# Optimization experiments

Hardware: AMD Instinct MI355X
Metric: run time of the kernel (lower is better)

The kernel has to match this reference:

```python
import jax, jax.numpy as jnp
import numpy as np
from jax import lax

NPOINT = 1024
NSAMPLE = 32
EPS = 1e-5


def setup_inputs() -> dict:
    key = jax.random.key(0)
    ks = jax.random.split(key, 8)
    B, N, CF = 16, 4096, 64
    xyz = jax.random.normal(ks[0], (B, N, 3), jnp.float32)
    points = jax.random.normal(ks[1], (B, N, CF), jnp.float32)
    in_ch = 3 + CF
    # 1x1 Conv2d weights stored as (out_ch, in_ch); kaiming-ish scale
    w0 = jax.random.normal(ks[2], (64, in_ch), jnp.float32) / np.sqrt(in_ch)
    w1 = jax.random.normal(ks[3], (64, 64), jnp.float32) / np.sqrt(64)
    w2 = jax.random.normal(ks[4], (128, 64), jnp.float32) / np.sqrt(64)
    z64 = jnp.zeros((64,), jnp.float32)
    z128 = jnp.zeros((128,), jnp.float32)
    o64 = jnp.ones((64,), jnp.float32)
    o128 = jnp.ones((128,), jnp.float32)
    return {
        "xyz": xyz, "points": points,
        "w0": w0, "b0": z64, "g0": o64, "bb0": z64,
        "w1": w1, "b1": z64, "g1": o64, "bb1": z64,
        "w2": w2, "b2": z128, "g2": o128, "bb2": z128,
    }


def _fps(xyz, npoint):
    """Iterative farthest point sampling. xyz: (B,N,3) -> (B,npoint) int32.
    Deterministic start at index 0 (torch uses a random start)."""
    B, N, _ = xyz.shape

    def step(carry, _):
        distance, farthest = carry
        centroid = jnp.take_along_axis(xyz, farthest[:, None, None], axis=1)  # (B,1,3)
        dist = jnp.sum((xyz - centroid) ** 2, -1)  # (B,N)
        distance = jnp.minimum(distance, dist)
        new_far = jnp.argmax(distance, axis=-1).astype(jnp.int32)
        return (distance, new_far), farthest

    init = (jnp.full((B, N), 1e10, xyz.dtype), jnp.zeros((B,), jnp.int32))
    _, cents = lax.scan(step, init, None, length=npoint)  # (npoint, B)
    return cents.T  # (B, npoint)


def _gather(pts, idx):
    """pts: (B,N,C), idx: (B,S,K) -> (B,S,K,C)"""
    return jax.vmap(lambda p, i: p[i])(pts, idx)


def _bn_relu(x, g, b):
    # training-mode BatchNorm over all axes except channel (last), biased var
    mean = jnp.mean(x, axis=(0, 1, 2))
    var = jnp.var(x, axis=(0, 1, 2))
    return jax.nn.relu(g * (x - mean) * lax.rsqrt(var + EPS) + b)


def reference(xyz, points, w0, b0, g0, bb0, w1, b1, g1, bb1, w2, b2, g2, bb2):
    B, N, _ = xyz.shape
    fps_idx = _fps(xyz, NPOINT)  # (B,S)
    new_xyz = jnp.take_along_axis(xyz, fps_idx[..., None], axis=1)  # (B,S,3)
    # squared distances centroid->all points: (B,S,N)
    d2 = (jnp.sum(new_xyz ** 2, -1)[:, :, None]
          + jnp.sum(xyz ** 2, -1)[:, None, :]
          - 2.0 * jnp.einsum("bsc,bnc->bsn", new_xyz, xyz))
    _, idx = lax.top_k(-d2, NSAMPLE)  # (B,S,K) nearest-K (sort-based ball query)
    grouped_xyz = _gather(xyz, idx) - new_xyz[:, :, None, :]  # (B,S,K,3)
    grouped_pts = _gather(points, idx)  # (B,S,K,CF)
    h = jnp.concatenate([grouped_xyz, grouped_pts], axis=-1)  # (B,S,K,3+CF)
    for w, b, g, bb in ((w0, b0, g0, bb0), (w1, b1, g1, bb1), (w2, b2, g2, bb2)):
        h = _bn_relu(jnp.einsum("bskc,oc->bsko", h, w) + b, g, bb)
    new_points = jnp.max(h, axis=2)  # (B,S,C_out) max over K
    new_points = jnp.transpose(new_points, (0, 2, 1))  # (B,C_out,S) matches torch
    return new_xyz, new_points
```

## Files before the change

### kernel.cpp

```cpp
#include <hip/hip_runtime.h>
#include <hip/hip_bf16.h>

#define NB 16
#define NN 4096
#define NS 1024
#define NK 32
#define CF 64
#define CIN 67
#define MTOT 524288
#define NEWP_OFF 49152

__device__ inline unsigned bf16bits(float v) {
    __hip_bfloat16 h = __float2bfloat16(v);
    unsigned short s;
    __builtin_memcpy(&s, &h, 2);
    return (unsigned)s;
}
__device__ inline float4 ldY4(const float* p) { return *(const float4*)p; }
__device__ inline float4 ldY4(const __hip_bfloat16* p) {
    ushort4 u = *(const ushort4*)p;
    return make_float4(__uint_as_float((unsigned)u.x << 16),
                       __uint_as_float((unsigned)u.y << 16),
                       __uint_as_float((unsigned)u.z << 16),
                       __uint_as_float((unsigned)u.w << 16));
}
__device__ inline void stY2(float* p, float a, float b) { *(float2*)p = make_float2(a, b); }
__device__ inline void stY2(__hip_bfloat16* p, float a, float b) {
    *(unsigned*)p = bf16bits(a) | (bf16bits(b) << 16);
}

template <int CTRL>
__device__ inline float dppredmax(float v) {
    int j = __builtin_amdgcn_update_dpp(__float_as_int(v), __float_as_int(v),
                                        CTRL, 0xF, 0xF, false);
    return fmaxf(v, __int_as_float(j));
}
template <int CTRL>
__device__ inline float dppredmin(float v) {
    int j = __builtin_amdgcn_update_dpp(__float_as_int(v), __float_as_int(v),
                                        CTRL, 0xF, 0xF, false);
    return fminf(v, __int_as_float(j));
}
template <int CTRL>
__device__ inline float dppadd0(float v) {
    int j = __builtin_amdgcn_update_dpp(0, __float_as_int(v), CTRL, 0xF, 0xF, true);
    return __fadd_rn(v, __int_as_float(j));
}
template <int CTRL>
__device__ inline unsigned long long dppredmin64(unsigned long long v) {
    int lo = (int)(unsigned)(v & 0xffffffffULL), hi = (int)(unsigned)(v >> 32);
    unsigned nlo = (unsigned)__builtin_amdgcn_update_dpp(lo, lo, CTRL, 0xF, 0xF, false);
    unsigned nhi = (unsigned)__builtin_amdgcn_update_dpp(hi, hi, CTRL, 0xF, 0xF, false);
    unsigned long long o = ((unsigned long long)nhi << 32) | nlo;
    return o < v ? o : v;
}
__device__ inline float wavemax_to_all(float tmax) {
    float g = tmax;
    g = dppredmax<0x111>(g);
    g = dppredmax<0x112>(g);
    g = dppredmax<0x114>(g);
    g = dppredmax<0x118>(g);
    g = dppredmax<0x142>(g);
    g = dppredmax<0x143>(g);
    return __int_as_float(__builtin_amdgcn_readlane(__float_as_int(g), 63));
}
__device__ inline unsigned long long wavemin64_to_all(unsigned long long v) {
    v = dppredmin64<0x111>(v);
    v = dppredmin64<0x112>(v);
    v = dppredmin64<0x114>(v);
    v = dppredmin64<0x118>(v);
    v = dppredmin64<0x142>(v);
    v = dppredmin64<0x143>(v);
    unsigned lo = (unsigned)__builtin_amdgcn_readlane((int)(unsigned)(v & 0xffffffffULL), 63);
    unsigned hi = (unsigned)__builtin_amdgcn_readlane((int)(unsigned)(v >> 32), 63);
    return ((unsigned long long)hi << 32) | lo;
}
__device__ inline float wavesum64(float v) {
    v = dppadd0<0x111>(v); v = dppadd0<0x112>(v);
    v = dppadd0<0x114>(v); v = dppadd0<0x118>(v);
    v = dppadd0<0x142>(v); v = dppadd0<0x143>(v);
    return v;
}
__device__ inline float segmax16(float v) {
    v = dppredmax<0x111>(v); v = dppredmax<0x112>(v);
    v = dppredmax<0x114>(v); v = dppredmax<0x118>(v);
    return v;
}
__device__ inline float segmin16(float v) {
    v = dppredmin<0x111>(v); v = dppredmin<0x112>(v);
    v = dppredmin<0x114>(v); v = dppredmin<0x118>(v);
    return v;
}

__global__ __launch_bounds__(256) void fps_kernel(const float* __restrict__ xyz,
                                                  int* __restrict__ fps_idx) {
    __shared__ float4 cpt[NN];
    __shared__ unsigned long long part[2][4];
    const int b = blockIdx.x, t = threadIdx.x;
    const float4* src = (const float4*)(xyz + (size_t)b * NN * 3);
    float px[16], py[16], pz[16], dist[16];
#pragma unroll
    for (int j = 0; j < 4; ++j) {
        float4 A = src[t * 12 + 3 * j], B4 = src[t * 12 + 3 * j + 1], C4 = src[t * 12 + 3 * j + 2];
        px[4 * j + 0] = A.x;  py[4 * j + 0] = A.y;  pz[4 * j + 0] = A.z;
        px[4 * j + 1] = A.w;  py[4 * j + 1] = B4.x; pz[4 * j + 1] = B4.y;
        px[4 * j + 2] = B4.z; py[4 * j + 2] = B4.w; pz[4 * j + 2] = C4.x;
        px[4 * j + 3] = C4.y; py[4 * j + 3] = C4.z; pz[4 * j + 3] = C4.w;
    }
#pragma unroll
    for (int i = 0; i < 16; ++i) {
        dist[i] = 1e10f;
        cpt[16 * t + i] = make_float4(px[i], py[i], pz[i], 0.f);
    }
    __syncthreads();
    int cur = 0;
    float4 c = cpt[0];
    const int wv = t >> 6;
    for (int s = 0; s < NS; ++s) {
        if (t == 0) fps_idx[(b << 10) + s] = cur;
#pragma unroll
        for (int i = 0; i < 16; ++i) {
            float dx = __fsub_rn(px[i], c.x), dy = __fsub_rn(py[i], c.y), dz = __fsub_rn(pz[i], c.z);
            float d = __fadd_rn(__fadd_rn(__fmul_rn(dx, dx), __fmul_rn(dy, dy)), __fmul_rn(dz, dz));
            dist[i] = fminf(dist[i], d);
        }
        float m0 = fmaxf(dist[0], dist[1]),   m1 = fmaxf(dist[2], dist[3]);
        float m2 = fmaxf(dist[4], dist[5]),   m3 = fmaxf(dist[6], dist[7]);
        float m4 = fmaxf(dist[8], dist[9]),   m5 = fmaxf(dist[10], dist[11]);
        float m6 = fmaxf(dist[12], dist[13]), m7 = fmaxf(dist[14], dist[15]);
        m0 = fmaxf(m0, m1); m2 = fmaxf(m2, m3); m4 = fmaxf(m4, m5); m6 = fmaxf(m6, m7);
        m0 = fmaxf(m0, m2); m4 = fmaxf(m4, m6);
        const float tmax = fmaxf(m0, m4);
        int mi = 15;
#pragma unroll
        for (int i = 14; i >= 0; --i) mi = (dist[i] == tmax) ? i : mi;
        const float gmax = wavemax_to_all(tmax);
        unsigned long long mask = __ballot(tmax == gmax);
        int ldr = __ffsll(mask) - 1;
        int widx = __builtin_amdgcn_readlane(16 * t + mi, ldr);
        if ((t & 63) == 0) {
            part[s & 1][wv] =
                ((unsigned long long)__float_as_uint(gmax) << 32) | (unsigned)(4095 - widx);
        }
        __syncthreads();
        unsigned long long k0 = part[s & 1][0], k1 = part[s & 1][1];
        unsigned long long k2 = part[s & 1][2], k3 = part[s & 1][3];
        unsigned long long ka = k0 > k1 ? k0 : k1, kb = k2 > k3 ? k2 : k3;
        unsigned long long k = ka > kb ? ka : kb;
        cur = 4095 - (int)(unsigned)(k & 0xffffffffu);
        c = cpt[cur];
    }
}

__global__ __launch_bounds__(256) void knn_kernel(const float* __restrict__ xyz,
                                                  const int* __restrict__ fps_idx,
                                                  int* __restrict__ knn,
                                                  float* __restrict__ out) {
    __shared__ float4 cpt[NN];
    const int b = blockIdx.x >> 5, cb = blockIdx.x & 31, t = threadIdx.x;
    for (int p = t; p < NN; p += 256) {
        const float* xr = xyz + ((size_t)(b << 12) + p) * 3;
        float x = xr[0], y = xr[1], z = xr[2];
        float pn = __fadd_rn(__fadd_rn(__fmul_rn(x, x), __fmul_rn(y, y)), __fmul_rn(z, z));
        cpt[p] = make_float4(x, y, z, pn);
    }
    __syncthreads();
    const int lane = t & 63, wv = t >> 6;
    for (int r = 0; r < 8; ++r) {
        const int s = (cb << 5) + (wv << 3) + r;
        const int ci = fps_idx[(b << 10) + s];
        const float4 cq = cpt[ci];
        const float cx = cq.x, cy = cq.y, cz = cq.z, cn = cq.w;
        if (lane < 3) out[((size_t)(b << 10) + s) * 3 + lane] = (lane == 0) ? cx : (lane == 1 ? cy : cz);
        unsigned long long m1 = ~0ULL, m2 = ~0ULL, m3 = ~0ULL;
#pragma unroll
        for (int i = 0; i < 64; ++i) {
            int p = lane + (i << 6);
            float4 q = cpt[p];
            float dot = __fadd_rn(__fadd_rn(__fmul_rn(cx, q.x), __fmul_rn(cy, q.y)),
                                  __fmul_rn(cz, q.z));
            float d2 = __fsub_rn(__fadd_rn(cn, q.w), __fmul_rn(2.0f, dot));
            unsigned u = __float_as_uint(d2);
            unsigned enc = u ^ ((unsigned)((int)u >> 31) | 0x80000000u);
            unsigned long long key = ((unsigned long long)enc << 32) | (unsigned)p;
            if (key < m3) {
                if (key < m1)      { m3 = m2; m2 = m1; m1 = key; }
                else if (key < m2) { m3 = m2; m2 = key; }
                else               { m3 = key; }
            }
        }
        unsigned myidx = 0;
        for (int j = 0; j < 32; ++j) {
            const unsigned long long vmin = wavemin64_to_all(m1);
            if (lane == j) myidx = (unsigned)(vmin & 0xffffffffu);
            if (m1 == vmin) {
                m1 = m2; m2 = m3; m3 = ~0ULL;
                if (m1 == ~0ULL) {
#pragma unroll
                    for (int i = 0; i < 64; ++i) {
                        int p = lane + (i << 6);
                        float4 q = cpt[p];
                        float dot = __fadd_rn(__fadd_rn(__fmul_rn(cx, q.x), __fmul_rn(cy, q.y)),
                                              __fmul_rn(cz, q.z));
                        float d2 = __fsub_rn(__fadd_rn(cn, q.w), __fmul_rn(2.0f, dot));
                        unsigned u = __float_as_uint(d2);
                        unsigned enc = u ^ ((unsigned)((int)u >> 31) | 0x80000000u);
                        unsigned long long key = ((unsigned long long)enc << 32) | (unsigned)p;
                        if (key > vmin && key < m3) {
                            if (key < m1)      { m3 = m2; m2 = m1; m1 = key; }
                            else if (key < m2) { m3 = m2; m2 = key; }
                            else               { m3 = key; }
                        }
                    }
                }
            }
        }
        const int rowbase = ((b << 10) + s) << 5;
        if (lane < 32) knn[rowbase + lane] = (int)myidx;
    }
}

template <typename YT>
__global__ __launch_bounds__(256) void conv0_kernel(
    const float* __restrict__ xyz, const float* __restrict__ points,
    const float* __restrict__ out_xyz, const int* __restrict__ knn,
    const float* __restrict__ w0, const float* __restrict__ b0,
    YT* __restrict__ Y0, float* __restrict__ gs, float* __restrict__ gq) {
    __shared__ float Ht[CIN][128];
    __shared__ float bsm[64], bqm[64];
    const int t = threadIdx.x;
    const int eb = blockIdx.x << 7;
    {
        const int le = t >> 1, part = t & 1;
        const int e = eb + le;
        const int b = e >> 15, s = (e >> 5) & 1023;
        const int pidx = knn[e];
        const float4* pr = (const float4*)(points + (((size_t)(b << 12) + pidx) << 6)) + (part << 3);
        if (part == 0) {
            const float* xr = xyz + ((size_t)(b << 12) + pidx) * 3;
            const float* cr = out_xyz + ((size_t)(b << 10) + s) * 3;
            Ht[0][le] = xr[0] - cr[0];
            Ht[1][le] = xr[1] - cr[1];
            Ht[2][le] = xr[2] - cr[2];
        }
#pragma unroll
        for (int q = 0; q < 8; ++q) {
            float4 v = pr[q];
            int c = 3 + (part << 5) + (q << 2);
            Ht[c][le] = v.x; Ht[c + 1][le] = v.y; Ht[c + 2][le] = v.z; Ht[c + 3][le] = v.w;
        }
    }
    __syncthreads();
    const int wvu = __builtin_amdgcn_readfirstlane(t >> 6);
    const int lane = t & 63, e2 = (t & 63) << 1;
    const float* __restrict__ wrow = w0 + (wvu << 4) * CIN;
    float acc[16][2];
#pragma unroll
    for (int i = 0; i < 16; ++i) { acc[i][0] = 0.f; acc[i][1] = 0.f; }
#pragma unroll 2
    for (int c = 0; c < CIN; ++c) {
        const float2 a = *(const float2*)&Ht[c][e2];
#pragma unroll
        for (int i = 0; i < 16; ++i) {
            const float w = wrow[i * CIN + c];
            acc[i][0] += w * a.x;
            acc[i][1] += w * a.y;
        }
    }
    const int o0 = wvu << 4;
#pragma unroll
    for (int i = 0; i < 16; ++i) {
        const float bi = b0[o0 + i];
        const float v0 = acc[i][0] + bi, v1 = acc[i][1] + bi;
        stY2(&Y0[(size_t)(o0 + i) * MTOT + eb + e2], v0, v1);
        float ss = wavesum64(v0 + v1);
        float qq = wavesum64(v0 * v0 + v1 * v1);
        if (lane == 63) { bsm[o0 + i] = ss; bqm[o0 + i] = qq; }
    }
    __syncthreads();
    if (t < 64) atomicAdd(&gs[t], bsm[t]);
    else if (t < 128) atomicAdd(&gq[t - 64], bqm[t - 64]);
}

template <typename YT>
__global__ __launch_bounds__(256) void conv1_kernel(
    const YT* __restrict__ Y0, const float* __restrict__ w1, const float* __restrict__ b1,
    const float* __restrict__ gsp, const float* __restrict__ gqp,
    const float* __restrict__ g, const float* __restrict__ bb,
    YT* __restrict__ Y1, float* __restrict__ gs, float* __restrict__ gq) {
    __shared__ float At[64][128];
    __shared__ float bnsc[64], bnsh[64];
    __shared__ float bsm[64], bqm[64];
    const int t = threadIdx.x;
    const int eb = blockIdx.x << 7;
    if (t < 64) {
        const float inv = 1.f / (float)MTOT;
        float mean = gsp[t] * inv;
        float var = gqp[t] * inv - mean * mean;
        float r = g[t] / sqrtf(var + 1e-5f);
        bnsc[t] = r; bnsh[t] = bb[t] - mean * r;
    }
    __syncthreads();
    {
        const int c = t >> 2, base = (t & 3) << 5;
        const float sx = bnsc[c], hx = bnsh[c];
#pragma unroll
        for (int q = 0; q < 8; ++q) {
            const int col = base + (q << 2);
            float4 y = ldY4(&Y0[(size_t)c * MTOT + eb + col]);
            *(float4*)&At[c][col] = make_float4(fmaxf(sx * y.x + hx, 0.f),
                                                fmaxf(sx * y.y + hx, 0.f),
                                                fmaxf(sx * y.z + hx, 0.f),
                                                fmaxf(sx * y.w + hx, 0.f));
        }
    }
    __syncthreads();
    const int wvu = __builtin_amdgcn_readfirstlane(t >> 6);
    const int lane = t & 63, e2 = (t & 63) << 1;
    const float* __restrict__ wrow = w1 + (wvu << 4) * 64;
    float acc[16][2];
#pragma unroll
    for (int i = 0; i < 16; ++i) { acc[i][0] = 0.f; acc[i][1] = 0.f; }
#pragma unroll 2
    for (int c = 0; c < 64; ++c) {
        const float2 a = *(const float2*)&At[c][e2];
#pragma unroll
        for (int i = 0; i < 16; ++i) {
            const float w = wrow[(i << 6) + c];
            acc[i][0] += w * a.x;
            acc[i][1] += w * a.y;
        }
    }
    const int o0 = wvu << 4;
#pragma unroll
    for (int i = 0; i < 16; ++i) {
        const float bi = b1[o0 + i];
        const float v0 = acc[i][0] + bi, v1 = acc[i][1] + bi;
        stY2(&Y1[(size_t)(o0 + i) * MTOT + eb + e2], v0, v1);
        float ss = wavesum64(v0 + v1);
        float qq = wavesum64(v0 * v0 + v1 * v1);
        if (lane == 63) { bsm[o0 + i] = ss; bqm[o0 + i] = qq; }
    }
    __syncthreads();
    if (t < 64) atomicAdd(&gs[t], bsm[t]);
    else if (t < 128) atomicAdd(&gq[t - 64], bqm[t - 64]);
}

template <typename YT>
__global__ __launch_bounds__(256) void conv2s_kernel(
    const YT* __restrict__ Y1, const float* __restrict__ w2, const float* __restrict__ b2,
    const float* __restrict__ gsp, const float* __restrict__ gqp,
    const float* __restrict__ g, const float* __restrict__ bb,
    float* __restrict__ gs, float* __restrict__ gq,
    float* __restrict__ Mx, float* __restrict__ Mn) {
    __shared__ float At[64][128];
    __shared__ float bnsc[64], bnsh[64];
    __shared__ float bsm[128], bqm[128];
    __shared__ float mxs[4][128], mns[4][128];
    const int t = threadIdx.x;
    const int eb = blockIdx.x << 7;
    if (t < 64) {
        const float inv = 1.f / (float)MTOT;
        float mean = gsp[t] * inv;
        float var = gqp[t] * inv - mean * mean;
        float r = g[t] / sqrtf(var + 1e-5f);
        bnsc[t] = r; bnsh[t] = bb[t] - mean * r;
    }
    __syncthreads();
    {
        const int c = t >> 2, base = (t & 3) << 5;
        const float sx = bnsc[c], hx = bnsh[c];
#pragma unroll
        for (int q = 0; q < 8; ++q) {
            const int col = base + (q << 2);
            float4 y = ldY4(&Y1[(size_t)c * MTOT + eb + col]);
            *(float4*)&At[c][col] = make_float4(fmaxf(sx * y.x + hx, 0.f),
                                                fmaxf(sx * y.y + hx, 0.f),
                                                fmaxf(sx * y.z + hx, 0.f),
                                                fmaxf(sx * y.w + hx, 0.f));
        }
    }
    __syncthreads();
    const int wvu = __builtin_amdgcn_readfirstlane(t >> 6);
    const int lane = t & 63, e2 = (t & 63) << 1;
    const float* __restrict__ wrow = w2 + (wvu << 5) * 64;
    float acc[32][2];
#pragma unroll
    for (int i = 0; i < 32; ++i) { acc[i][0] = 0.f; acc[i][1] = 0.f; }
#pragma unroll 2
    for (int c = 0; c < 64; ++c) {
        const float2 a = *(const float2*)&At[c][e2];
#pragma unroll
        for (int i = 0; i < 32; ++i) {
            const float w = wrow[(i << 6) + c];
            acc[i][0] += w * a.x;
            acc[i][1] += w * a.y;
        }
    }
    const int o0 = wvu << 5;
    const int srow = lane >> 4;
#pragma unroll
    for (int i = 0; i < 32; ++i) {
        const float bi = b2[o0 + i];
        const float v0 = acc[i][0] + bi, v1 = acc[i][1] + bi;
        float ss = wavesum64(v0 + v1);
        float qq = wavesum64(v0 * v0 + v1 * v1);
        if (lane == 63) { bsm[o0 + i] = ss; bqm[o0 + i] = qq; }
        float mx = segmax16(fmaxf(v0, v1));
        float mn = segmin16(fminf(v0, v1));
        if ((lane & 15) == 15) { mxs[srow][o0 + i] = mx; mns[srow][o0 + i] = mn; }
    }
    __syncthreads();
    if (t < 128) atomicAdd(&gs[t], bsm[t]);
    else atomicAdd(&gq[t - 128], bqm[t - 128]);
    const int sidx0 = blockIdx.x << 2;
    for (int i = t; i < 512; i += 256) {
        int row = i >> 7, o = i & 127;
        Mx[(size_t)(sidx0 + row) * 128 + o] = mxs[row][o];
        Mn[(size_t)(sidx0 + row) * 128 + o] = mns[row][o];
    }
}

__global__ __launch_bounds__(256) void final2_kernel(
    const float* __restrict__ Mx, const float* __restrict__ Mn,
    const float* __restrict__ gsp, const float* __restrict__ gqp,
    const float* __restrict__ g, const float* __restrict__ bb,
    float* __restrict__ out) {
    __shared__ float T[128][65];
    __shared__ float bnsc[128], bnsh[128];
    const int t = threadIdx.x;
    if (t < 128) {
        const float inv = 1.f / (float)MTOT;
        float mean = gsp[t] * inv;
        float var = gqp[t] * inv - mean * mean;
        float r = g[t] / sqrtf(var + 1e-5f);
        bnsc[t] = r; bnsh[t] = bb[t] - mean * r;
    }
    __syncthreads();
    const int b = blockIdx.x >> 4, s0 = (blockIdx.x & 15) << 6;
    for (int i = t; i < 8192; i += 256) {
        int r = i >> 7, o = i & 127;
        size_t src = ((size_t)(b << 10) + s0 + r) * 128 + o;
        float a = bnsc[o];
        float m = (a >= 0.f) ? Mx[src] : Mn[src];
        T[o][r] = fmaxf(a * m + bnsh[o], 0.f);
    }
    __syncthreads();
    float* np = out + NEWP_OFF;
    for (int i = t; i < 8192; i += 256) {
        int o = i >> 6, r = i & 63;
        np[((size_t)(b << 7) + o) * 1024 + s0 + r] = T[o][r];
    }
}

extern "C" void kernel_launch(void* const* d_in, const int* in_sizes, int n_in,
                              void* d_out, int out_size, void* d_ws, size_t ws_size,
                              hipStream_t stream) {
    const float* xyz = (const float*)d_in[0];
    const float* points = (const float*)d_in[1];
    const float* w0 = (const float*)d_in[2];
    const float* b0 = (const float*)d_in[3];
    const float* g0 = (const float*)d_in[4];
    const float* bb0 = (const float*)d_in[5];
    const float* w1 = (const float*)d_in[6];
    const float* b1 = (const float*)d_in[7];
    const float* g1 = (const float*)d_in[8];
    const float* bb1 = (const float*)d_in[9];
    const float* w2 = (const float*)d_in[10];
    const float* b2 = (const float*)d_in[11];
    const float* g2 = (const float*)d_in[12];
    const float* bb2 = (const float*)d_in[13];
    float* out = (float*)d_out;
    char* ws = (char*)d_ws;

    int* knn = (int*)(ws);
    int* fps = (int*)(ws + (2u << 20));
    float* stats = (float*)(ws + (2u << 20) + (1u << 16));
    float *gs0 = stats, *gq0 = stats + 64, *gs1 = stats + 128, *gq1 = stats + 192;
    float *gs2 = stats + 256, *gq2 = stats + 384;
    float* Mx = (float*)(ws + (4ull << 20));
    float* Mn = (float*)(ws + (12ull << 20));
    const size_t yoff = 20ull << 20;
    const size_t ybytes_f32 = (size_t)MTOT * 64 * 4;
    const bool f32p = ws_size >= yoff + 2 * ybytes_f32;

    (void)hipMemsetAsync(stats, 0, 512 * sizeof(float), stream);
    fps_kernel<<<NB, 256, 0, stream>>>(xyz, fps);
    knn_kernel<<<NB * 32, 256, 0, stream>>>(xyz, fps, knn, out);

    if (f32p) {
        float* Y0 = (float*)(ws + yoff);
        float* Y1 = Y0 + (size_t)MTOT * 64;
        conv0_kernel<float><<<4096, 256, 0, stream>>>(xyz, points, out, knn, w0, b0, Y0, gs0, gq0);
        conv1_kernel<float><<<4096, 256, 0, stream>>>(Y0, w1, b1, gs0, gq0, g0, bb0, Y1, gs1, gq1);
        conv2s_kernel<float><<<4096, 256, 0, stream>>>(Y1, w2, b2, gs1, gq1, g1, bb1, gs2, gq2, Mx, Mn);
    } else {
        __hip_bfloat16* Y0 = (__hip_bfloat16*)(ws + yoff);
        __hip_bfloat16* Y1 = Y0 + (size_t)MTOT * 64;
        conv0_kernel<__hip_bfloat16><<<4096, 256, 0, stream>>>(xyz, points, out, knn, w0, b0, Y0, gs0, gq0);
        conv1_kernel<__hip_bfloat16><<<4096, 256, 0, stream>>>(Y0, w1, b1, gs0, gq0, g0, bb0, Y1, gs1, gq1);
        conv2s_kernel<__hip_bfloat16><<<4096, 256, 0, stream>>>(Y1, w2, b2, gs1, gq1, g1, bb1, gs2, gq2, Mx, Mn);
    }
    final2_kernel<<<256, 256, 0, stream>>>(Mx, Mn, gs2, gq2, g2, bb2, out);
}
```

Measured before the change: 1.313 ms.

## Process two batches per FPS block to interleave independent serial chains

The FPS kernel now runs two batch elements in one 256-thread block, launching 8 blocks instead of 16. The two independent distance updates and argmax reductions are interleaved so their latency chains overlap and they share one barrier per step. This doubles registers and LDS per block (two 64KB point buffers) and halves the number of blocks, so each step does twice the ALU work on the same CU.

```diff
diff --git a/kernel.cpp b/kernel.cpp
--- a/kernel.cpp
+++ b/kernel.cpp
@@ -92,63 +92,108 @@
     return v;
 }
 
-__global__ __launch_bounds__(256) void fps_kernel(const float* __restrict__ xyz,
-                                                  int* __restrict__ fps_idx) {
-    __shared__ float4 cpt[NN];
-    __shared__ unsigned long long part[2][4];
-    const int b = blockIdx.x, t = threadIdx.x;
-    const float4* src = (const float4*)(xyz + (size_t)b * NN * 3);
-    float px[16], py[16], pz[16], dist[16];
+__global__ __launch_bounds__(256, 1) void fps_kernel(const float* __restrict__ xyz,
+                                                     int* __restrict__ fps_idx) {
+    __shared__ float4 cptA[NN];
+    __shared__ float4 cptB[NN];
+    __shared__ unsigned long long partA[2][4], partB[2][4];
+    const int bA = blockIdx.x, bB = blockIdx.x + 8, t = threadIdx.x;
+    const float4* srcA = (const float4*)(xyz + (size_t)bA * NN * 3);
+    const float4* srcB = (const float4*)(xyz + (size_t)bB * NN * 3);
+    float pxA[16], pyA[16], pzA[16], dA[16];
+    float pxB[16], pyB[16], pzB[16], dB[16];
 #pragma unroll
     for (int j = 0; j < 4; ++j) {
-        float4 A = src[t * 12 + 3 * j], B4 = src[t * 12 + 3 * j + 1], C4 = src[t * 12 + 3 * j + 2];
-        px[4 * j + 0] = A.x;  py[4 * j + 0] = A.y;  pz[4 * j + 0] = A.z;
-        px[4 * j + 1] = A.w;  py[4 * j + 1] = B4.x; pz[4 * j + 1] = B4.y;
-        px[4 * j + 2] = B4.z; py[4 * j + 2] = B4.w; pz[4 * j + 2] = C4.x;
-        px[4 * j + 3] = C4.y; py[4 * j + 3] = C4.z; pz[4 * j + 3] = C4.w;
+        float4 A = srcA[t * 12 + 3 * j], B4 = srcA[t * 12 + 3 * j + 1], C4 = srcA[t * 12 + 3 * j + 2];
+        pxA[4 * j + 0] = A.x;  pyA[4 * j + 0] = A.y;  pzA[4 * j + 0] = A.z;
+        pxA[4 * j + 1] = A.w;  pyA[4 * j + 1] = B4.x; pzA[4 * j + 1] = B4.y;
+        pxA[4 * j + 2] = B4.z; pyA[4 * j + 2] = B4.w; pzA[4 * j + 2] = C4.x;
+        pxA[4 * j + 3] = C4.y; pyA[4 * j + 3] = C4.z; pzA[4 * j + 3] = C4.w;
+    }
+#pragma unroll
+    for (int j = 0; j < 4; ++j) {
+        float4 A = srcB[t * 12 + 3 * j], B4 = srcB[t * 12 + 3 * j + 1], C4 = srcB[t * 12 + 3 * j + 2];
+        pxB[4 * j + 0] = A.x;  pyB[4 * j + 0] = A.y;  pzB[4 * j + 0] = A.z;
+        pxB[4 * j + 1] = A.w;  pyB[4 * j + 1] = B4.x; pzB[4 * j + 1] = B4.y;
+        pxB[4 * j + 2] = B4.z; pyB[4 * j + 2] = B4.w; pzB[4 * j + 2] = C4.x;
+        pxB[4 * j + 3] = C4.y; pyB[4 * j + 3] = C4.z; pzB[4 * j + 3] = C4.w;
     }
 #pragma unroll
     for (int i = 0; i < 16; ++i) {
-        dist[i] = 1e10f;
-        cpt[16 * t + i] = make_float4(px[i], py[i], pz[i], 0.f);
-    }
-    __syncthreads();
-    int cur = 0;
-    float4 c = cpt[0];
+        dA[i] = 1e10f; dB[i] = 1e10f;
+        cptA[16 * t + i] = make_float4(pxA[i], pyA[i], pzA[i], 0.f);
+        cptB[16 * t + i] = make_float4(pxB[i], pyB[i], pzB[i], 0.f);
+    }
+    __syncthreads();
+    int curA = 0, curB = 0;
+    float4 cA = cptA[0], cB = cptB[0];
     const int wv = t >> 6;
     for (int s = 0; s < NS; ++s) {
-        if (t == 0) fps_idx[(b << 10) + s] = cur;
+        if (t == 0) {
+            fps_idx[(bA << 10) + s] = curA;
+            fps_idx[(bB << 10) + s] = curB;
+        }
 #pragma unroll
         for (int i = 0; i < 16; ++i) {
-            float dx = __fsub_rn(px[i], c.x), dy = __fsub_rn(py[i], c.y), dz = __fsub_rn(pz[i], c.z);
+            float dx = __fsub_rn(pxA[i], cA.x), dy = __fsub_rn(pyA[i], cA.y), dz = __fsub_rn(pzA[i], cA.z);
             float d = __fadd_rn(__fadd_rn(__fmul_rn(dx, dx), __fmul_rn(dy, dy)), __fmul_rn(dz, dz));
-            dist[i] = fminf(dist[i], d);
-        }
-        float m0 = fmaxf(dist[0], dist[1]),   m1 = fmaxf(dist[2], dist[3]);
-        float m2 = fmaxf(dist[4], dist[5]),   m3 = fmaxf(dist[6], dist[7]);
-        float m4 = fmaxf(dist[8], dist[9]),   m5 = fmaxf(dist[10], dist[11]);
-        float m6 = fmaxf(dist[12], dist[13]), m7 = fmaxf(dist[14], dist[15]);
-        m0 = fmaxf(m0, m1); m2 = fmaxf(m2, m3); m4 = fmaxf(m4, m5); m6 = fmaxf(m6, m7);
-        m0 = fmaxf(m0, m2); m4 = fmaxf(m4, m6);
-        const float tmax = fmaxf(m0, m4);
-        int mi = 15;
-#pragma unroll
-        for (int i = 14; i >= 0; --i) mi = (dist[i] == tmax) ? i : mi;
-        const float gmax = wavemax_to_all(tmax);
-        unsigned long long mask = __ballot(tmax == gmax);
-        int ldr = __ffsll(mask) - 1;
-        int widx = __builtin_amdgcn_readlane(16 * t + mi, ldr);
+            dA[i] = fminf(dA[i], d);
+        }
+#pragma unroll
+        for (int i = 0; i < 16; ++i) {
+            float dx = __fsub_rn(pxB[i], cB.x), dy = __fsub_rn(pyB[i], cB.y), dz = __fsub_rn(pzB[i], cB.z);
+            float d = __fadd_rn(__fadd_rn(__fmul_rn(dx, dx), __fmul_rn(dy, dy)), __fmul_rn(dz, dz));
+            dB[i] = fminf(dB[i], d);
+        }
+        float a0 = fmaxf(dA[0], dA[1]),   a1 = fmaxf(dA[2], dA[3]);
+        float a2 = fmaxf(dA[4], dA[5]),   a3 = fmaxf(dA[6], dA[7]);
+        float a4 = fmaxf(dA[8], dA[9]),   a5 = fmaxf(dA[10], dA[11]);
+        float a6 = fmaxf(dA[12], dA[13]), a7 = fmaxf(dA[14], dA[15]);
+        a0 = fmaxf(a0, a1); a2 = fmaxf(a2, a3); a4 = fmaxf(a4, a5); a6 = fmaxf(a6, a7);
+        a0 = fmaxf(a0, a2); a4 = fmaxf(a4, a6);
+        const float tmaxA = fmaxf(a0, a4);
+        int miA = 15;
+#pragma unroll
+        for (int i = 14; i >= 0; --i) miA = (dA[i] == tmaxA) ? i : miA;
+        float b0 = fmaxf(dB[0], dB[1]),   b1 = fmaxf(dB[2], dB[3]);
+        float b2 = fmaxf(dB[4], dB[5]),   b3 = fmaxf(dB[6], dB[7]);
+        float b4 = fmaxf(dB[8], dB[9]),   b5 = fmaxf(dB[10], dB[11]);
+        float b6 = fmaxf(dB[12], dB[13]), b7 = fmaxf(dB[14], dB[15]);
+        b0 = fmaxf(b0, b1); b2 = fmaxf(b2, b3); b4 = fmaxf(b4, b5); b6 = fmaxf(b6, b7);
+        b0 = fmaxf(b0, b2); b4 = fmaxf(b4, b6);
+        const float tmaxB = fmaxf(b0, b4);
+        int miB = 15;
+#pragma unroll
+        for (int i = 14; i >= 0; --i) miB = (dB[i] == tmaxB) ? i : miB;
+        const float gA = wavemax_to_all(tmaxA);
+        const float gB = wavemax_to_all(tmaxB);
+        unsigned long long mA = __ballot(tmaxA == gA);
+        unsigned long long mB = __ballot(tmaxB == gB);
+        int widxA = __builtin_amdgcn_readlane(16 * t + miA, __ffsll(mA) - 1);
+        int widxB = __builtin_amdgcn_readlane(16 * t + miB, __ffsll(mB) - 1);
         if ((t & 63) == 0) {
-            part[s & 1][wv] =
-                ((unsigned long long)__float_as_uint(gmax) << 32) | (unsigned)(4095 - widx);
+            partA[s & 1][wv] =
+                ((unsigned long long)__float_as_uint(gA) << 32) | (unsigned)(4095 - widxA);
+            partB[s & 1][wv] =
+                ((unsigned long long)__float_as_uint(gB) << 32) | (unsigned)(4095 - widxB);
         }
         __syncthreads();
-        unsigned long long k0 = part[s & 1][0], k1 = part[s & 1][1];
-        unsigned long long k2 = part[s & 1][2], k3 = part[s & 1][3];
-        unsigned long long ka = k0 > k1 ? k0 : k1, kb = k2 > k3 ? k2 : k3;
-        unsigned long long k = ka > kb ? ka : kb;
-        cur = 4095 - (int)(unsigned)(k & 0xffffffffu);
-        c = cpt[cur];
+        {
+            unsigned long long k0 = partA[s & 1][0], k1 = partA[s & 1][1];
+            unsigned long long k2 = partA[s & 1][2], k3 = partA[s & 1][3];
+            unsigned long long ka = k0 > k1 ? k0 : k1, kb = k2 > k3 ? k2 : k3;
+            unsigned long long k = ka > kb ? ka : kb;
+            curA = 4095 - (int)(unsigned)(k & 0xffffffffu);
+        }
+        {
+            unsigned long long k0 = partB[s & 1][0], k1 = partB[s & 1][1];
+            unsigned long long k2 = partB[s & 1][2], k3 = partB[s & 1][3];
+            unsigned long long ka = k0 > k1 ? k0 : k1, kb = k2 > k3 ? k2 : k3;
+            unsigned long long k = ka > kb ? ka : kb;
+            curB = 4095 - (int)(unsigned)(k & 0xffffffffu);
+        }
+        cA = cptA[curA];
+        cB = cptB[curB];
     }
 }
 
@@ -485,7 +530,7 @@
     const bool f32p = ws_size >= yoff + 2 * ybytes_f32;
 
     (void)hipMemsetAsync(stats, 0, 512 * sizeof(float), stream);
-    fps_kernel<<<NB, 256, 0, stream>>>(xyz, fps);
+    fps_kernel<<<NB / 2, 256, 0, stream>>>(xyz, fps);
     knn_kernel<<<NB * 32, 256, 0, stream>>>(xyz, fps, knn, out);
 
     if (f32p) {
```

After: 1.737 ms. +32.3%, slower.
